# Kernel tuning notes

Hardware: AMD Instinct MI355X
Metric: run time of the kernel (lower is better)

Reference implementation:

```python
import jax, jax.numpy as jnp
import numpy as np
from math import log2

N_QUBITS = 11
N_LAYERS = 2
DEGREE = 3
N_TIMESTEPS = 8
BSZ = 64
DIM = 2 ** N_QUBITS
N_ROTS = 4 * N_QUBITS * N_LAYERS  # 88


def _ry(theta):
    # batched RY(theta): (B,) -> (B,2,2) complex64
    h = 0.5 * theta
    c, s = jnp.cos(h), jnp.sin(h)
    U = jnp.stack([jnp.stack([c, -s], -1), jnp.stack([s, c], -1)], -2)
    return U.astype(jnp.complex64)


def _rx(theta):
    # batched RX(theta): (B,) -> (B,2,2) complex64
    h = 0.5 * theta
    c = jnp.cos(h).astype(jnp.complex64)
    s = (-1j) * jnp.sin(h).astype(jnp.complex64)
    return jnp.stack([jnp.stack([c, s], -1), jnp.stack([s, c], -1)], -2)


def _apply_1q(state, U, w):
    # state: (B,) + (2,)*n ; apply per-batch 2x2 U on wire w
    s = jnp.moveaxis(state, w + 1, 1)
    shp = s.shape
    s = s.reshape(shp[0], 2, -1)
    s = jnp.einsum('bij,bjr->bir', U, s)
    return jnp.moveaxis(s.reshape(shp), 1, w + 1)


def _apply_crx(state, theta, c_w, t_w):
    # controlled-RX: apply RX on target wire t_w where control wire c_w is |1>
    U = _rx(theta)
    s = jnp.moveaxis(state, (c_w + 1, t_w + 1), (1, 2))
    shp = s.shape
    s = s.reshape(shp[0], 2, 2, -1)
    s1 = jnp.einsum('bij,bjr->bir', U, s[:, 1])
    s = jnp.concatenate([s[:, :1], s1[:, None]], axis=1).reshape(shp)
    return jnp.moveaxis(s, (1, 2), (c_w + 1, t_w + 1))


def _sim14_evolve(state, params):
    # faithful sim14_circuit (v3 fixed RY-CRX gate set), batched angles
    n = state.ndim - 1
    layers = params.shape[1] // (4 * n)
    idx = 0
    for _ in range(layers):
        for i in range(n):
            state = _apply_1q(state, _ry(params[:, idx]), i); idx += 1
        for i in range(n - 1, -1, -1):
            state = _apply_crx(state, params[:, idx], i, (i + 1) % n); idx += 1
        for i in range(n):
            state = _apply_1q(state, _ry(params[:, idx]), i); idx += 1
        for i in [n - 1] + list(range(n - 1)):
            state = _apply_crx(state, params[:, idx], i, (i - 1) % n); idx += 1
    return state


def _apply_unitaries(base, uparams, coeffs):
    # apply_unitaries_pl: repeat_interleave + evolve + LCU einsum
    bsz, T, n_rots = uparams.shape
    dim = base.shape[1]
    n = int(round(log2(dim)))
    flat = uparams.reshape(bsz * T, n_rots)
    rep = jnp.repeat(base, T, axis=0).reshape((bsz * T,) + (2,) * n)
    ev = _sim14_evolve(rep, flat).reshape(bsz, T, dim)
    return jnp.einsum('bti,bt->bi', ev, coeffs.astype(jnp.complex64))


def setup_inputs() -> dict:
    key = jax.random.key(0)
    k1, k2, k3, k4 = jax.random.split(key, 4)
    base_states = jax.random.normal(k1, (BSZ, DIM), dtype=jnp.float32)
    unitary_params = jax.random.normal(k2, (BSZ, N_TIMESTEPS, N_ROTS), dtype=jnp.float32)
    lcu_coeffs = jax.random.normal(k3, (BSZ, N_TIMESTEPS), dtype=jnp.float32)
    poly_coeffs = jax.random.normal(k4, (DEGREE + 1,), dtype=jnp.float32)
    return {"base_states": base_states, "unitary_params": unitary_params,
            "lcu_coeffs": lcu_coeffs, "poly_coeffs": poly_coeffs}


def reference(base_states, unitary_params, lcu_coeffs, poly_coeffs):
    # evaluate_polynomial_state_pl (QSVT polynomial state preparation)
    base = base_states.astype(jnp.complex64)
    base = base / jnp.linalg.norm(base, axis=1, keepdims=True)  # valid quantum state
    pc = poly_coeffs.astype(jnp.complex64)
    acc = pc[0] * base
    working = base
    for k in range(1, poly_coeffs.shape[0]):
        working = _apply_unitaries(working, unitary_params, lcu_coeffs)
        acc = acc + pc[k] * working
    out = acc / jnp.sum(jnp.abs(poly_coeffs)).astype(jnp.complex64)
    # return real/imag stacked so output is real-valued: (bsz, dim, 2)
    return jnp.stack([out.real, out.imag], axis=-1)
```

## Files before the change

### kernel.cpp

```cpp
#include <hip/hip_runtime.h>
#include <utility>

#define DIM 2048
#define NQ 11
#define NROT 88
#define BSZ 64
#define NT 8
#define NPC 4

#if __has_builtin(__builtin_amdgcn_permlane16_swap)
#define HAVE_PL16 1
#else
#define HAVE_PL16 0
#endif
#if __has_builtin(__builtin_amdgcn_permlane32_swap)
#define HAVE_PL32 1
#else
#define HAVE_PL32 0
#endif

constexpr int g_type(int G) {
    int j = G % 44;
    return (j < 11 || (j >= 22 && j < 33)) ? 0 : 1;
}
constexpr int g_pt(int G) {
    int j = G % 44;
    if (j < 11) return 10 - j;
    if (j < 22) { int i = 21 - j; int tw = (i + 1 == NQ) ? 0 : i + 1; return 10 - tw; }
    if (j < 33) return 10 - (j - 22);
    if (j == 33) return 1;
    int i = j - 34; int tw = (i + 10) % NQ; return 10 - tw;
}
constexpr int g_pcb(int G) {
    int j = G % 44;
    if (j >= 11 && j < 22) { int i = 21 - j; return 10 - i; }
    if (j == 33) return 0;
    if (j >= 34) { int i = j - 34; return 10 - i; }
    return -1;
}
constexpr bool use_sum_tier(int lb) {
    return (lb == 4 && HAVE_PL16) || (lb == 5 && HAVE_PL32);
}

constexpr int tmap(int b) {
    if (b == 2) return 8;  if (b == 8) return 2;
    if (b == 3) return 9;  if (b == 9) return 3;
    if (b == 5) return 10; if (b == 10) return 5;
    return b;
}

constexpr int lop_j(int k) {
    if (k < 8)  return 3 + k;
    if (k == 8) return -1;
    if (k < 12) return k - 9;
    if (k == 12) return 11;
    if (k == 13) return -1;
    if (k < 22) return 12 + (k - 14);
    if (k == 22) return -1;
    if (k == 23) return 20;
    if (k == 24) return 21;
    if (k < 31) { int w[6] = {0, 1, 2, 3, 9, 10}; return 22 + w[k - 25]; }
    if (k < 36) return 33 + (k - 31);
    if (k == 36) return -1;
    if (k < 42) return 26 + (k - 37);
    return 38 + (k - 42);
}
constexpr bool lop_B(int k) {
    return (k >= 9 && k <= 12) || (k >= 23 && k <= 35);
}
constexpr int lop_tpar(int k) { return (k == 8 || k == 22) ? 0 : 1; }

template<int G>
__device__ __forceinline__ void get_cs(float c0, float s0, float c1, float s1,
                                       float& c, float& s) {
    if constexpr (G < 64) {
        c = __int_as_float(__builtin_amdgcn_readlane(__float_as_int(c0), G));
        s = __int_as_float(__builtin_amdgcn_readlane(__float_as_int(s0), G));
    } else {
        c = __int_as_float(__builtin_amdgcn_readlane(__float_as_int(c1), G - 64));
        s = __int_as_float(__builtin_amdgcn_readlane(__float_as_int(s1), G - 64));
    }
}

template<int LB>
__device__ __forceinline__ float lxp(float x) {
    if constexpr (LB == 0) {
        return __int_as_float(__builtin_amdgcn_update_dpp(
            __float_as_int(x), __float_as_int(x), 0xB1, 0xF, 0xF, true));
    } else if constexpr (LB == 1) {
        return __int_as_float(__builtin_amdgcn_update_dpp(
            __float_as_int(x), __float_as_int(x), 0x4E, 0xF, 0xF, true));
    } else if constexpr (LB == 2) {
        return __int_as_float(__builtin_amdgcn_ds_swizzle(__float_as_int(x), 0x101F));
    } else if constexpr (LB == 3) {
        return __int_as_float(__builtin_amdgcn_update_dpp(
            __float_as_int(x), __float_as_int(x), 0x128, 0xF, 0xF, true));
    } else if constexpr (LB == 4) {
        return __int_as_float(__builtin_amdgcn_ds_swizzle(__float_as_int(x), 0x401F));
    } else {
        return __shfl_xor(x, 32, 64);
    }
}

template<int LB>
__device__ __forceinline__ float lxsum(float x) {
#if HAVE_PL16
    if constexpr (LB == 4) {
        unsigned u = __float_as_uint(x);
        auto r = __builtin_amdgcn_permlane16_swap(u, u, false, false);
        return __uint_as_float(r[0]) + __uint_as_float(r[1]);
    }
#endif
#if HAVE_PL32
    if constexpr (LB == 5) {
        unsigned u = __float_as_uint(x);
        auto r = __builtin_amdgcn_permlane32_swap(u, u, false, false);
        return __uint_as_float(r[0]) + __uint_as_float(r[1]);
    }
#endif
    return x + lxp<LB>(x);
}

template<int G, bool PB>
__device__ __forceinline__ void apply_gate(
    float2 (&R)[2], float2 (&I)[2],
    float c0, float s0, float c1, float s1,
    float4* __restrict__ exbuf, const int tid)
{
    constexpr int type = g_type(G);
    constexpr int pt0  = g_pt(G);
    constexpr int pcb0 = g_pcb(G);
    constexpr int pt   = PB ? tmap(pt0) : pt0;
    constexpr int pcb  = (pcb0 < 0) ? -1 : (PB ? tmap(pcb0) : pcb0);
    float c, s;
    get_cs<G>(c0, s0, c1, s1, c, s);

    if constexpr (pt == 0) {
        if constexpr (type == 0) {
#pragma unroll
            for (int m = 0; m < 2; ++m) {
                float er = R[m].x, orr = R[m].y, ei = I[m].x, oi = I[m].y;
                R[m].x = c*er - s*orr;  R[m].y = s*er + c*orr;
                I[m].x = c*ei - s*oi;   I[m].y = s*ei + c*oi;
            }
        } else if constexpr (pcb == 1) {
            float er = R[1].x, orr = R[1].y, ei = I[1].x, oi = I[1].y;
            R[1].x = c*er + s*oi;   I[1].x = c*ei - s*orr;
            R[1].y = c*orr + s*ei;  I[1].y = c*oi - s*er;
        } else {
            const bool ctrl = (tid >> (pcb - 2)) & 1;
            if (ctrl) {
#pragma unroll
                for (int m = 0; m < 2; ++m) {
                    float er = R[m].x, orr = R[m].y, ei = I[m].x, oi = I[m].y;
                    R[m].x = c*er + s*oi;   I[m].x = c*ei - s*orr;
                    R[m].y = c*orr + s*ei;  I[m].y = c*oi - s*er;
                }
            }
        }
    } else if constexpr (pt == 1) {
        if constexpr (type == 0) {
            float2 l = R[0], h = R[1], li = I[0], hi = I[1];
            R[0].x = c*l.x - s*h.x;   R[0].y = c*l.y - s*h.y;
            R[1].x = s*l.x + c*h.x;   R[1].y = s*l.y + c*h.y;
            I[0].x = c*li.x - s*hi.x; I[0].y = c*li.y - s*hi.y;
            I[1].x = s*li.x + c*hi.x; I[1].y = s*li.y + c*hi.y;
        } else if constexpr (pcb == 0) {
            float lr = R[0].y, li = I[0].y, hr = R[1].y, hi = I[1].y;
            R[0].y = c*lr + s*hi;   I[0].y = c*li - s*hr;
            R[1].y = c*hr + s*li;   I[1].y = c*hi - s*lr;
        } else {
            const bool ctrl = (tid >> (pcb - 2)) & 1;
            if (ctrl) {
                float2 l = R[0], h = R[1], li = I[0], hi = I[1];
                R[0].x = c*l.x + s*hi.x;  R[0].y = c*l.y + s*hi.y;
                I[0].x = c*li.x - s*h.x;  I[0].y = c*li.y - s*h.y;
                R[1].x = c*h.x + s*li.x;  R[1].y = c*h.y + s*li.y;
                I[1].x = c*hi.x - s*l.x;  I[1].y = c*hi.y - s*l.y;
            }
        }
    } else if constexpr (pt <= 7) {
        constexpr int lb = pt - 2;
        if constexpr (use_sum_tier(lb)) {
            if constexpr (type == 0) {
                const float sg = ((tid >> lb) & 1) ? s : -s;
                const float k1 = c - sg;
#pragma unroll
                for (int m = 0; m < 2; ++m) {
                    float srx = lxsum<lb>(R[m].x), sry = lxsum<lb>(R[m].y);
                    float six = lxsum<lb>(I[m].x), siy = lxsum<lb>(I[m].y);
                    R[m].x = k1*R[m].x + sg*srx;  R[m].y = k1*R[m].y + sg*sry;
                    I[m].x = k1*I[m].x + sg*six;  I[m].y = k1*I[m].y + sg*siy;
                }
            } else if constexpr (pcb == 0) {
#pragma unroll
                for (int m = 0; m < 2; ++m) {
                    float sR = lxsum<lb>(R[m].y), sI = lxsum<lb>(I[m].y);
                    float r = R[m].y, i = I[m].y;
                    R[m].y = c*r - s*i + s*sI;
                    I[m].y = c*i + s*r - s*sR;
                }
            } else if constexpr (pcb == 1) {
                float sRx = lxsum<lb>(R[1].x), sRy = lxsum<lb>(R[1].y);
                float sIx = lxsum<lb>(I[1].x), sIy = lxsum<lb>(I[1].y);
                float rx = R[1].x, ry = R[1].y, ix = I[1].x, iy = I[1].y;
                R[1].x = c*rx - s*ix + s*sIx;  R[1].y = c*ry - s*iy + s*sIy;
                I[1].x = c*ix + s*rx - s*sRx;  I[1].y = c*iy + s*ry - s*sRy;
            } else {
                const bool ctrl = (tid >> (pcb - 2)) & 1;
                if (ctrl) {
#pragma unroll
                    for (int m = 0; m < 2; ++m) {
                        float sRx = lxsum<lb>(R[m].x), sRy = lxsum<lb>(R[m].y);
                        float sIx = lxsum<lb>(I[m].x), sIy = lxsum<lb>(I[m].y);
                        float rx = R[m].x, ry = R[m].y, ix = I[m].x, iy = I[m].y;
                        R[m].x = c*rx - s*ix + s*sIx;  R[m].y = c*ry - s*iy + s*sIy;
                        I[m].x = c*ix + s*rx - s*sRx;  I[m].y = c*iy + s*ry - s*sRy;
                    }
                }
            }
        } else {
            if constexpr (type == 0) {
                const float sg = ((tid >> lb) & 1) ? s : -s;
#pragma unroll
                for (int m = 0; m < 2; ++m) {
                    float prx = lxp<lb>(R[m].x), pry = lxp<lb>(R[m].y);
                    float pix = lxp<lb>(I[m].x), piy = lxp<lb>(I[m].y);
                    R[m].x = c*R[m].x + sg*prx;  R[m].y = c*R[m].y + sg*pry;
                    I[m].x = c*I[m].x + sg*pix;  I[m].y = c*I[m].y + sg*piy;
                }
            } else if constexpr (pcb == 0) {
#pragma unroll
                for (int m = 0; m < 2; ++m) {
                    float pry = lxp<lb>(R[m].y), piy = lxp<lb>(I[m].y);
                    R[m].y = c*R[m].y + s*piy;
                    I[m].y = c*I[m].y - s*pry;
                }
            } else if constexpr (pcb == 1) {
                float prx = lxp<lb>(R[1].x), pry = lxp<lb>(R[1].y);
                float pix = lxp<lb>(I[1].x), piy = lxp<lb>(I[1].y);
                R[1].x = c*R[1].x + s*pix;  R[1].y = c*R[1].y + s*piy;
                I[1].x = c*I[1].x - s*prx;  I[1].y = c*I[1].y - s*pry;
            } else {
                const bool ctrl = (tid >> (pcb - 2)) & 1;
                if (ctrl) {
#pragma unroll
                    for (int m = 0; m < 2; ++m) {
                        float prx = lxp<lb>(R[m].x), pry = lxp<lb>(R[m].y);
                        float pix = lxp<lb>(I[m].x), piy = lxp<lb>(I[m].y);
                        R[m].x = c*R[m].x + s*pix;  R[m].y = c*R[m].y + s*piy;
                        I[m].x = c*I[m].x - s*prx;  I[m].y = c*I[m].y - s*pry;
                    }
                }
            }
        }
    }
}

__device__ __forceinline__ int swz(int s) { return s ^ ((s >> 7) & 7); }

template<int PAR>
__device__ __forceinline__ void transpose_swap(float2 (&R)[2], float2 (&I)[2],
                                               float4* __restrict__ exbuf, const int tid)
{
    float4* buf = exbuf + PAR * 1024;
    const int d06 = ((tid >> 0) ^ (tid >> 6)) & 1;
    const int d17 = ((tid >> 1) ^ (tid >> 7)) & 1;
    const int d38 = ((tid >> 3) ^ (tid >> 8)) & 1;
    const int q = tid ^ (d06 * 65) ^ (d17 * 130) ^ (d38 * 264);
    buf[swz(tid * 2 + 0)] = make_float4(R[0].x, R[0].y, I[0].x, I[0].y);
    buf[swz(tid * 2 + 1)] = make_float4(R[1].x, R[1].y, I[1].x, I[1].y);
    __syncthreads();
    float4 v0 = buf[swz(q * 2 + 0)];
    float4 v1 = buf[swz(q * 2 + 1)];
    R[0] = make_float2(v0.x, v0.y); I[0] = make_float2(v0.z, v0.w);
    R[1] = make_float2(v1.x, v1.y); I[1] = make_float2(v1.z, v1.w);
}

template<int K>
__device__ __forceinline__ void apply_op(
    float2 (&R)[2], float2 (&I)[2],
    float c0, float s0, float c1, float s1,
    float4* __restrict__ exbuf, const int tid)
{
    constexpr int layer = K / 48;
    constexpr int k = K % 48;
    constexpr int j = lop_j(k);
    if constexpr (j < 0) {
        transpose_swap<lop_tpar(k)>(R, I, exbuf, tid);
    } else {
        apply_gate<layer * 44 + j, lop_B(k)>(R, I, c0, s0, c1, s1, exbuf, tid);
    }
}

template<int... Ks>
__device__ __forceinline__ void apply_all(std::integer_sequence<int, Ks...>,
    float2 (&R)[2], float2 (&I)[2],
    float c0, float s0, float c1, float s1,
    float4* __restrict__ exbuf, const int tid)
{
    (apply_op<Ks>(R, I, c0, s0, c1, s1, exbuf, tid), ...);
}

template<int MODE>
__global__ __launch_bounds__(512, 4) void evolve_kernel(
    const void* __restrict__ src, const float* __restrict__ uparams,
    const float* __restrict__ lcu, float2* __restrict__ pout,
    const float* __restrict__ pcoef, float2* __restrict__ acc, int kprev)
{
    __shared__ float4 exbuf[2048];
    __shared__ float red[9];

    const int b = blockIdx.x >> 3;
    const int t = blockIdx.x & 7;
    const int tid = threadIdx.x;
    const int lane = tid & 63;

    const float* __restrict__ th_row = uparams + (size_t)(b * NT + t) * NROT;
    float th0 = 0.5f * th_row[lane];
    float th1 = (lane < NROT - 64) ? 0.5f * th_row[64 + lane] : 0.f;
    float tc0 = cosf(th0), ts0 = sinf(th0);
    float tc1 = cosf(th1), ts1 = sinf(th1);

    float2 R[2], I[2];
    if constexpr (MODE == 0) {
        const float4* b4 = (const float4*)((const float*)src + (size_t)b * DIM);
        float4 v = b4[tid];
        float loc = v.x*v.x + v.y*v.y + v.z*v.z + v.w*v.w;
        for (int off = 32; off > 0; off >>= 1) loc += __shfl_down(loc, off, 64);
        if ((tid & 63) == 0) red[tid >> 6] = loc;
        __syncthreads();
        if (tid == 0) { float sm = 0.f; for (int w = 0; w < 8; ++w) sm += red[w]; red[8] = sm; }
        __syncthreads();
        const float inv = rsqrtf(red[8]);
        R[0] = make_float2(v.x * inv, v.y * inv);
        R[1] = make_float2(v.z * inv, v.w * inv);
        I[0] = make_float2(0.f, 0.f);
        I[1] = make_float2(0.f, 0.f);
        if (t == 0) {
            const float p0 = pcoef[0];
            float4* a4 = (float4*)(acc + (size_t)b * DIM);
            a4[tid*2+0] = make_float4(p0*R[0].x, 0.f, p0*R[0].y, 0.f);
            a4[tid*2+1] = make_float4(p0*R[1].x, 0.f, p0*R[1].y, 0.f);
        }
    } else if constexpr (MODE == 1) {
        R[0] = R[1] = I[0] = I[1] = make_float2(0.f, 0.f);
        const float2* s2 = (const float2*)src;
        for (int cc = 0; cc < NT; ++cc) {
            const float4* p4 = (const float4*)(s2 + ((size_t)b * NT + cc) * DIM);
#pragma unroll
            for (int m = 0; m < 2; ++m) {
                float4 v = p4[tid*2+m];
                R[m].x += v.x; I[m].x += v.y; R[m].y += v.z; I[m].y += v.w;
            }
        }
        if (t == 0) {
            const float pk = pcoef[kprev];
            float4* a4 = (float4*)(acc + (size_t)b * DIM);
#pragma unroll
            for (int m = 0; m < 2; ++m) {
                float4 v = a4[tid*2+m];
                v.x += pk * R[m].x; v.y += pk * I[m].x;
                v.z += pk * R[m].y; v.w += pk * I[m].y;
                a4[tid*2+m] = v;
            }
        }
    } else {
        const float2* s2 = (const float2*)src;
        const float4* p4 = (const float4*)(s2 + (size_t)b * DIM);
#pragma unroll
        for (int m = 0; m < 2; ++m) {
            float4 v = p4[tid*2+m];
            R[m].x = v.x; I[m].x = v.y; R[m].y = v.z; I[m].y = v.w;
        }
    }

    apply_all(std::make_integer_sequence<int, 96>{}, R, I,
              tc0, ts0, tc1, ts1, exbuf, tid);

    const float coeff = lcu[b * NT + t];
    float4* o4 = (float4*)(pout + ((size_t)b * NT + t) * DIM);
#pragma unroll
    for (int m = 0; m < 2; ++m)
        o4[tid*2+m] = make_float4(coeff*R[m].x, coeff*I[m].x, coeff*R[m].y, coeff*I[m].y);
}

__global__ __launch_bounds__(256) void final_kernel(
    const float2* __restrict__ partial, const float* __restrict__ pcoef,
    const float2* __restrict__ acc, float* __restrict__ out)
{
    int b = blockIdx.x >> 3;
    int i = ((blockIdx.x & 7) << 8) | threadIdx.x;
    float sr = 0.f, si = 0.f;
    for (int c = 0; c < NT; ++c) {
        float2 v = partial[((size_t)b * NT + c) * DIM + i];
        sr += v.x; si += v.y;
    }
    float sabs = 0.f;
    for (int q = 0; q < NPC; ++q) sabs += fabsf(pcoef[q]);
    float invn = 1.0f / sabs;
    float pk = pcoef[NPC - 1];
    float2 a = acc[(size_t)b * DIM + i];
    out[((size_t)b * DIM + i) * 2 + 0] = (a.x + pk * sr) * invn;
    out[((size_t)b * DIM + i) * 2 + 1] = (a.y + pk * si) * invn;
}

__global__ __launch_bounds__(256) void setup_kernel(
    const float* __restrict__ base, const float* __restrict__ pc,
    float2* __restrict__ working, float2* __restrict__ acc)
{
    int b = blockIdx.x;
    int tid = threadIdx.x;
    __shared__ float red[4];
    float ssum = 0.f;
    for (int i = tid; i < DIM; i += 256) {
        float v = base[b * DIM + i];
        ssum += v * v;
    }
    for (int off = 32; off > 0; off >>= 1) ssum += __shfl_down(ssum, off, 64);
    if ((tid & 63) == 0) red[tid >> 6] = ssum;
    __syncthreads();
    if (tid == 0) red[0] = red[0] + red[1] + red[2] + red[3];
    __syncthreads();
    float inv = rsqrtf(red[0]);
    float p0 = pc[0];
    for (int i = tid; i < DIM; i += 256) {
        float v = base[b * DIM + i] * inv;
        working[b * DIM + i] = make_float2(v, 0.f);
        acc[b * DIM + i] = make_float2(p0 * v, 0.f);
    }
}

__global__ __launch_bounds__(256) void reduce_kernel(
    const float2* __restrict__ partial, const float* __restrict__ pcoef,
    float2* __restrict__ working, float2* __restrict__ acc,
    float* __restrict__ out, int k, int last)
{
    int b = blockIdx.x >> 3;
    int i = ((blockIdx.x & 7) << 8) | threadIdx.x;
    float pk = pcoef[k];
    float sr = 0.f, si = 0.f;
    for (int c = 0; c < NT; ++c) {
        float2 v = partial[((size_t)b * NT + c) * DIM + i];
        sr += v.x; si += v.y;
    }
    working[b * DIM + i] = make_float2(sr, si);
    float2 a = acc[b * DIM + i];
    a.x += pk * sr; a.y += pk * si;
    acc[b * DIM + i] = a;
    if (last) {
        float sabs = 0.f;
        for (int q = 0; q < NPC; ++q) sabs += fabsf(pcoef[q]);
        float invn = 1.0f / sabs;
        out[((size_t)b * DIM + i) * 2 + 0] = a.x * invn;
        out[((size_t)b * DIM + i) * 2 + 1] = a.y * invn;
    }
}

extern "C" void kernel_launch(void* const* d_in, const int* in_sizes, int n_in,
                              void* d_out, int out_size, void* d_ws, size_t ws_size,
                              hipStream_t stream) {
    const float* base = (const float*)d_in[0];
    const float* upar = (const float*)d_in[1];
    const float* lcu  = (const float*)d_in[2];
    const float* pc   = (const float*)d_in[3];
    float* out = (float*)d_out;

    const size_t plane = (size_t)BSZ * DIM * sizeof(float2);
    char* ws = (char*)d_ws;

    if (ws_size >= (1 + 3 * (size_t)NT) * plane) {
        float2* acc = (float2*)ws;
        float2* pA  = (float2*)(ws + plane);
        float2* pB  = (float2*)(ws + plane + (size_t)NT * plane);
        float2* pC  = (float2*)(ws + plane + (size_t)2 * NT * plane);
        evolve_kernel<0><<<BSZ * NT, 512, 0, stream>>>(base, upar, lcu, pA, pc, acc, 0);
        evolve_kernel<1><<<BSZ * NT, 512, 0, stream>>>(pA,   upar, lcu, pB, pc, acc, 1);
        evolve_kernel<1><<<BSZ * NT, 512, 0, stream>>>(pB,   upar, lcu, pC, pc, acc, 2);
        final_kernel<<<BSZ * 8, 256, 0, stream>>>(pC, pc, acc, out);
    } else {
        float2* working = (float2*)ws;
        float2* acc     = (float2*)(ws + plane);
        float2* pA      = (float2*)(ws + 2 * plane);
        setup_kernel<<<BSZ, 256, 0, stream>>>(base, pc, working, acc);
        for (int k = 1; k <= NPC - 1; ++k) {
            evolve_kernel<2><<<BSZ * NT, 512, 0, stream>>>(working, upar, lcu, pA, pc, acc, 0);
            reduce_kernel<<<BSZ * 8, 256, 0, stream>>>(pA, pc, working, acc, out,
                                                       k, (k == NPC - 1) ? 1 : 0);
        }
    }
}
```

Baseline: 85.24 us.

## Use 1024 threads per state with one amplitude pair each and 4-bit transposes

Each evolve block now runs 1024 threads, each holding one complex pair instead of two. The qubit-to-lane mapping, the transpose schedule (now three shared-memory transposes per layer with a 16-way swizzle) and the gate dispatch are all rebuilt to match. The aim is more parallelism per state and less register pressure per thread, so cross-lane gate work gets spread over more wavefronts. The cost is an extra transpose and barrier per layer, plus more block-wide synchronisation across 16 waves.

```diff
diff --git a/kernel.cpp b/kernel.cpp
--- a/kernel.cpp
+++ b/kernel.cpp
@@ -43,32 +43,37 @@
 }
 
 constexpr int tmap(int b) {
-    if (b == 2) return 8;  if (b == 8) return 2;
-    if (b == 3) return 9;  if (b == 9) return 3;
-    if (b == 5) return 10; if (b == 10) return 5;
+    if (b >= 1 && b <= 4) return b + 6;
+    if (b >= 7 && b <= 10) return b - 6;
     return b;
 }
 
 constexpr int lop_j(int k) {
-    if (k < 8)  return 3 + k;
-    if (k == 8) return -1;
-    if (k < 12) return k - 9;
+    if (k < 7)  return 4 + k;
+    if (k == 7) return -1;
+    if (k < 12) return k - 8;
     if (k == 12) return 11;
     if (k == 13) return -1;
-    if (k < 22) return 12 + (k - 14);
-    if (k == 22) return -1;
-    if (k == 23) return 20;
-    if (k == 24) return 21;
-    if (k < 31) { int w[6] = {0, 1, 2, 3, 9, 10}; return 22 + w[k - 25]; }
-    if (k < 36) return 33 + (k - 31);
-    if (k == 36) return -1;
-    if (k < 42) return 26 + (k - 37);
-    return 38 + (k - 42);
+    if (k < 21) return 12 + (k - 14);
+    if (k == 21) return -1;
+    if (k < 25) return 19 + (k - 22);
+    if (k < 29) return 22 + (k - 25);
+    if (k == 29) return 26;
+    if (k == 30) return 27;
+    if (k == 31) return 32;
+    if (k == 32) return -1;
+    if (k < 37) return 28 + (k - 33);
+    if (k == 37) return 33;
+    if (k == 38) return 34;
+    if (k == 39) return -1;
+    if (k < 46) return 35 + (k - 40);
+    if (k == 46) return -1;
+    return 41 + (k - 47);
 }
 constexpr bool lop_B(int k) {
-    return (k >= 9 && k <= 12) || (k >= 23 && k <= 35);
-}
-constexpr int lop_tpar(int k) { return (k == 8 || k == 22) ? 0 : 1; }
+    return (k >= 8 && k <= 12) || (k >= 22 && k <= 31) || (k >= 40 && k <= 45);
+}
+constexpr int lop_tpar(int k) { return (k == 7 || k == 21 || k == 39) ? 0 : 1; }
 
 template<int G>
 __device__ __forceinline__ void get_cs(float c0, float s0, float c1, float s1,
@@ -122,180 +127,114 @@
 }
 
 template<int G, bool PB>
-__device__ __forceinline__ void apply_gate(
-    float2 (&R)[2], float2 (&I)[2],
-    float c0, float s0, float c1, float s1,
-    float4* __restrict__ exbuf, const int tid)
+__device__ __forceinline__ void apply_gate(float2& R, float2& I,
+    float c0, float s0, float c1, float s1, const int tid)
 {
     constexpr int type = g_type(G);
-    constexpr int pt0  = g_pt(G);
+    constexpr int pt   = PB ? tmap(g_pt(G)) : g_pt(G);
     constexpr int pcb0 = g_pcb(G);
-    constexpr int pt   = PB ? tmap(pt0) : pt0;
     constexpr int pcb  = (pcb0 < 0) ? -1 : (PB ? tmap(pcb0) : pcb0);
+    static_assert(pt <= 6, "block-bit target must run in transposed layout");
     float c, s;
     get_cs<G>(c0, s0, c1, s1, c, s);
 
     if constexpr (pt == 0) {
         if constexpr (type == 0) {
-#pragma unroll
-            for (int m = 0; m < 2; ++m) {
-                float er = R[m].x, orr = R[m].y, ei = I[m].x, oi = I[m].y;
-                R[m].x = c*er - s*orr;  R[m].y = s*er + c*orr;
-                I[m].x = c*ei - s*oi;   I[m].y = s*ei + c*oi;
+            float rx = R.x, ry = R.y, ix = I.x, iy = I.y;
+            R.x = c*rx - s*ry;  R.y = s*rx + c*ry;
+            I.x = c*ix - s*iy;  I.y = s*ix + c*iy;
+        } else {
+            const bool ctrl = (tid >> (pcb - 1)) & 1;
+            if (ctrl) {
+                float rx = R.x, ry = R.y, ix = I.x, iy = I.y;
+                R.x = c*rx + s*iy;   I.x = c*ix - s*ry;
+                R.y = c*ry + s*ix;   I.y = c*iy - s*rx;
             }
-        } else if constexpr (pcb == 1) {
-            float er = R[1].x, orr = R[1].y, ei = I[1].x, oi = I[1].y;
-            R[1].x = c*er + s*oi;   I[1].x = c*ei - s*orr;
-            R[1].y = c*orr + s*ei;  I[1].y = c*oi - s*er;
-        } else {
-            const bool ctrl = (tid >> (pcb - 2)) & 1;
-            if (ctrl) {
-#pragma unroll
-                for (int m = 0; m < 2; ++m) {
-                    float er = R[m].x, orr = R[m].y, ei = I[m].x, oi = I[m].y;
-                    R[m].x = c*er + s*oi;   I[m].x = c*ei - s*orr;
-                    R[m].y = c*orr + s*ei;  I[m].y = c*oi - s*er;
-                }
-            }
-        }
-    } else if constexpr (pt == 1) {
-        if constexpr (type == 0) {
-            float2 l = R[0], h = R[1], li = I[0], hi = I[1];
-            R[0].x = c*l.x - s*h.x;   R[0].y = c*l.y - s*h.y;
-            R[1].x = s*l.x + c*h.x;   R[1].y = s*l.y + c*h.y;
-            I[0].x = c*li.x - s*hi.x; I[0].y = c*li.y - s*hi.y;
-            I[1].x = s*li.x + c*hi.x; I[1].y = s*li.y + c*hi.y;
-        } else if constexpr (pcb == 0) {
-            float lr = R[0].y, li = I[0].y, hr = R[1].y, hi = I[1].y;
-            R[0].y = c*lr + s*hi;   I[0].y = c*li - s*hr;
-            R[1].y = c*hr + s*li;   I[1].y = c*hi - s*lr;
-        } else {
-            const bool ctrl = (tid >> (pcb - 2)) & 1;
-            if (ctrl) {
-                float2 l = R[0], h = R[1], li = I[0], hi = I[1];
-                R[0].x = c*l.x + s*hi.x;  R[0].y = c*l.y + s*hi.y;
-                I[0].x = c*li.x - s*h.x;  I[0].y = c*li.y - s*h.y;
-                R[1].x = c*h.x + s*li.x;  R[1].y = c*h.y + s*li.y;
-                I[1].x = c*hi.x - s*l.x;  I[1].y = c*hi.y - s*l.y;
-            }
-        }
-    } else if constexpr (pt <= 7) {
-        constexpr int lb = pt - 2;
+        }
+    } else {
+        constexpr int lb = pt - 1;
         if constexpr (use_sum_tier(lb)) {
             if constexpr (type == 0) {
                 const float sg = ((tid >> lb) & 1) ? s : -s;
                 const float k1 = c - sg;
-#pragma unroll
-                for (int m = 0; m < 2; ++m) {
-                    float srx = lxsum<lb>(R[m].x), sry = lxsum<lb>(R[m].y);
-                    float six = lxsum<lb>(I[m].x), siy = lxsum<lb>(I[m].y);
-                    R[m].x = k1*R[m].x + sg*srx;  R[m].y = k1*R[m].y + sg*sry;
-                    I[m].x = k1*I[m].x + sg*six;  I[m].y = k1*I[m].y + sg*siy;
-                }
+                float srx = lxsum<lb>(R.x), sry = lxsum<lb>(R.y);
+                float six = lxsum<lb>(I.x), siy = lxsum<lb>(I.y);
+                R.x = k1*R.x + sg*srx;  R.y = k1*R.y + sg*sry;
+                I.x = k1*I.x + sg*six;  I.y = k1*I.y + sg*siy;
             } else if constexpr (pcb == 0) {
-#pragma unroll
-                for (int m = 0; m < 2; ++m) {
-                    float sR = lxsum<lb>(R[m].y), sI = lxsum<lb>(I[m].y);
-                    float r = R[m].y, i = I[m].y;
-                    R[m].y = c*r - s*i + s*sI;
-                    I[m].y = c*i + s*r - s*sR;
-                }
-            } else if constexpr (pcb == 1) {
-                float sRx = lxsum<lb>(R[1].x), sRy = lxsum<lb>(R[1].y);
-                float sIx = lxsum<lb>(I[1].x), sIy = lxsum<lb>(I[1].y);
-                float rx = R[1].x, ry = R[1].y, ix = I[1].x, iy = I[1].y;
-                R[1].x = c*rx - s*ix + s*sIx;  R[1].y = c*ry - s*iy + s*sIy;
-                I[1].x = c*ix + s*rx - s*sRx;  I[1].y = c*iy + s*ry - s*sRy;
+                float sry = lxsum<lb>(R.y), siy = lxsum<lb>(I.y);
+                float ry = R.y, iy = I.y;
+                R.y = c*ry - s*iy + s*siy;
+                I.y = c*iy + s*ry - s*sry;
             } else {
-                const bool ctrl = (tid >> (pcb - 2)) & 1;
+                const bool ctrl = (tid >> (pcb - 1)) & 1;
                 if (ctrl) {
-#pragma unroll
-                    for (int m = 0; m < 2; ++m) {
-                        float sRx = lxsum<lb>(R[m].x), sRy = lxsum<lb>(R[m].y);
-                        float sIx = lxsum<lb>(I[m].x), sIy = lxsum<lb>(I[m].y);
-                        float rx = R[m].x, ry = R[m].y, ix = I[m].x, iy = I[m].y;
-                        R[m].x = c*rx - s*ix + s*sIx;  R[m].y = c*ry - s*iy + s*sIy;
-                        I[m].x = c*ix + s*rx - s*sRx;  I[m].y = c*iy + s*ry - s*sRy;
-                    }
+                    float srx = lxsum<lb>(R.x), sry = lxsum<lb>(R.y);
+                    float six = lxsum<lb>(I.x), siy = lxsum<lb>(I.y);
+                    float rx = R.x, ry = R.y, ix = I.x, iy = I.y;
+                    R.x = c*rx - s*ix + s*six;  R.y = c*ry - s*iy + s*siy;
+                    I.x = c*ix + s*rx - s*srx;  I.y = c*iy + s*ry - s*sry;
                 }
             }
         } else {
             if constexpr (type == 0) {
                 const float sg = ((tid >> lb) & 1) ? s : -s;
-#pragma unroll
-                for (int m = 0; m < 2; ++m) {
-                    float prx = lxp<lb>(R[m].x), pry = lxp<lb>(R[m].y);
-                    float pix = lxp<lb>(I[m].x), piy = lxp<lb>(I[m].y);
-                    R[m].x = c*R[m].x + sg*prx;  R[m].y = c*R[m].y + sg*pry;
-                    I[m].x = c*I[m].x + sg*pix;  I[m].y = c*I[m].y + sg*piy;
-                }
+                float prx = lxp<lb>(R.x), pry = lxp<lb>(R.y);
+                float pix = lxp<lb>(I.x), piy = lxp<lb>(I.y);
+                R.x = c*R.x + sg*prx;  R.y = c*R.y + sg*pry;
+                I.x = c*I.x + sg*pix;  I.y = c*I.y + sg*piy;
             } else if constexpr (pcb == 0) {
-#pragma unroll
-                for (int m = 0; m < 2; ++m) {
-                    float pry = lxp<lb>(R[m].y), piy = lxp<lb>(I[m].y);
-                    R[m].y = c*R[m].y + s*piy;
-                    I[m].y = c*I[m].y - s*pry;
-                }
-            } else if constexpr (pcb == 1) {
-                float prx = lxp<lb>(R[1].x), pry = lxp<lb>(R[1].y);
-                float pix = lxp<lb>(I[1].x), piy = lxp<lb>(I[1].y);
-                R[1].x = c*R[1].x + s*pix;  R[1].y = c*R[1].y + s*piy;
-                I[1].x = c*I[1].x - s*prx;  I[1].y = c*I[1].y - s*pry;
+                float pry = lxp<lb>(R.y), piy = lxp<lb>(I.y);
+                R.y = c*R.y + s*piy;
+                I.y = c*I.y - s*pry;
             } else {
-                const bool ctrl = (tid >> (pcb - 2)) & 1;
+                const bool ctrl = (tid >> (pcb - 1)) & 1;
                 if (ctrl) {
-#pragma unroll
-                    for (int m = 0; m < 2; ++m) {
-                        float prx = lxp<lb>(R[m].x), pry = lxp<lb>(R[m].y);
-                        float pix = lxp<lb>(I[m].x), piy = lxp<lb>(I[m].y);
-                        R[m].x = c*R[m].x + s*pix;  R[m].y = c*R[m].y + s*piy;
-                        I[m].x = c*I[m].x - s*prx;  I[m].y = c*I[m].y - s*pry;
-                    }
+                    float prx = lxp<lb>(R.x), pry = lxp<lb>(R.y);
+                    float pix = lxp<lb>(I.x), piy = lxp<lb>(I.y);
+                    R.x = c*R.x + s*pix;  R.y = c*R.y + s*piy;
+                    I.x = c*I.x - s*prx;  I.y = c*I.y - s*pry;
                 }
             }
         }
     }
 }
 
-__device__ __forceinline__ int swz(int s) { return s ^ ((s >> 7) & 7); }
+__device__ __forceinline__ int swz16(int s) { return s ^ ((s >> 6) & 15); }
 
 template<int PAR>
-__device__ __forceinline__ void transpose_swap(float2 (&R)[2], float2 (&I)[2],
-                                               float4* __restrict__ exbuf, const int tid)
+__device__ __forceinline__ void transpose_swap(float2& R, float2& I,
+    float4* __restrict__ exbuf, const int tid)
 {
     float4* buf = exbuf + PAR * 1024;
-    const int d06 = ((tid >> 0) ^ (tid >> 6)) & 1;
-    const int d17 = ((tid >> 1) ^ (tid >> 7)) & 1;
-    const int d38 = ((tid >> 3) ^ (tid >> 8)) & 1;
-    const int q = tid ^ (d06 * 65) ^ (d17 * 130) ^ (d38 * 264);
-    buf[swz(tid * 2 + 0)] = make_float4(R[0].x, R[0].y, I[0].x, I[0].y);
-    buf[swz(tid * 2 + 1)] = make_float4(R[1].x, R[1].y, I[1].x, I[1].y);
+    const int lo = tid & 15;
+    const int hi = (tid >> 6) & 15;
+    const int q = (tid & 0x030) | hi | (lo << 6);
+    buf[swz16(tid)] = make_float4(R.x, R.y, I.x, I.y);
     __syncthreads();
-    float4 v0 = buf[swz(q * 2 + 0)];
-    float4 v1 = buf[swz(q * 2 + 1)];
-    R[0] = make_float2(v0.x, v0.y); I[0] = make_float2(v0.z, v0.w);
-    R[1] = make_float2(v1.x, v1.y); I[1] = make_float2(v1.z, v1.w);
+    float4 v = buf[swz16(q)];
+    R = make_float2(v.x, v.y);
+    I = make_float2(v.z, v.w);
 }
 
 template<int K>
-__device__ __forceinline__ void apply_op(
-    float2 (&R)[2], float2 (&I)[2],
+__device__ __forceinline__ void apply_op(float2& R, float2& I,
     float c0, float s0, float c1, float s1,
     float4* __restrict__ exbuf, const int tid)
 {
-    constexpr int layer = K / 48;
-    constexpr int k = K % 48;
+    constexpr int layer = K / 50;
+    constexpr int k = K % 50;
     constexpr int j = lop_j(k);
     if constexpr (j < 0) {
         transpose_swap<lop_tpar(k)>(R, I, exbuf, tid);
     } else {
-        apply_gate<layer * 44 + j, lop_B(k)>(R, I, c0, s0, c1, s1, exbuf, tid);
+        apply_gate<layer * 44 + j, lop_B(k)>(R, I, c0, s0, c1, s1, tid);
     }
 }
 
 template<int... Ks>
 __device__ __forceinline__ void apply_all(std::integer_sequence<int, Ks...>,
-    float2 (&R)[2], float2 (&I)[2],
+    float2& R, float2& I,
     float c0, float s0, float c1, float s1,
     float4* __restrict__ exbuf, const int tid)
 {
@@ -303,13 +242,13 @@
 }
 
 template<int MODE>
-__global__ __launch_bounds__(512, 4) void evolve_kernel(
+__global__ __launch_bounds__(1024, 8) void evolve_kernel(
     const void* __restrict__ src, const float* __restrict__ uparams,
     const float* __restrict__ lcu, float2* __restrict__ pout,
     const float* __restrict__ pcoef, float2* __restrict__ acc, int kprev)
 {
     __shared__ float4 exbuf[2048];
-    __shared__ float red[9];
+    __shared__ float red[16];
 
     const int b = blockIdx.x >> 3;
     const int t = blockIdx.x & 7;
@@ -322,67 +261,54 @@
     float tc0 = cosf(th0), ts0 = sinf(th0);
     float tc1 = cosf(th1), ts1 = sinf(th1);
 
-    float2 R[2], I[2];
+    float2 R, I;
     if constexpr (MODE == 0) {
-        const float4* b4 = (const float4*)((const float*)src + (size_t)b * DIM);
-        float4 v = b4[tid];
-        float loc = v.x*v.x + v.y*v.y + v.z*v.z + v.w*v.w;
+        const float2* b2s = (const float2*)((const float*)src + (size_t)b * DIM);
+        float2 v = b2s[tid];
+        float loc = v.x * v.x + v.y * v.y;
         for (int off = 32; off > 0; off >>= 1) loc += __shfl_down(loc, off, 64);
-        if ((tid & 63) == 0) red[tid >> 6] = loc;
+        if (lane == 0) red[tid >> 6] = loc;
         __syncthreads();
-        if (tid == 0) { float sm = 0.f; for (int w = 0; w < 8; ++w) sm += red[w]; red[8] = sm; }
-        __syncthreads();
-        const float inv = rsqrtf(red[8]);
-        R[0] = make_float2(v.x * inv, v.y * inv);
-        R[1] = make_float2(v.z * inv, v.w * inv);
-        I[0] = make_float2(0.f, 0.f);
-        I[1] = make_float2(0.f, 0.f);
+        float tot = 0.f;
+#pragma unroll
+        for (int w = 0; w < 16; ++w) tot += red[w];
+        const float inv = rsqrtf(tot);
+        R = make_float2(v.x * inv, v.y * inv);
+        I = make_float2(0.f, 0.f);
         if (t == 0) {
             const float p0 = pcoef[0];
             float4* a4 = (float4*)(acc + (size_t)b * DIM);
-            a4[tid*2+0] = make_float4(p0*R[0].x, 0.f, p0*R[0].y, 0.f);
-            a4[tid*2+1] = make_float4(p0*R[1].x, 0.f, p0*R[1].y, 0.f);
+            a4[tid] = make_float4(p0 * R.x, 0.f, p0 * R.y, 0.f);
         }
     } else if constexpr (MODE == 1) {
-        R[0] = R[1] = I[0] = I[1] = make_float2(0.f, 0.f);
+        R = make_float2(0.f, 0.f); I = make_float2(0.f, 0.f);
         const float2* s2 = (const float2*)src;
         for (int cc = 0; cc < NT; ++cc) {
             const float4* p4 = (const float4*)(s2 + ((size_t)b * NT + cc) * DIM);
-#pragma unroll
-            for (int m = 0; m < 2; ++m) {
-                float4 v = p4[tid*2+m];
-                R[m].x += v.x; I[m].x += v.y; R[m].y += v.z; I[m].y += v.w;
-            }
+            float4 v = p4[tid];
+            R.x += v.x; I.x += v.y; R.y += v.z; I.y += v.w;
         }
         if (t == 0) {
             const float pk = pcoef[kprev];
             float4* a4 = (float4*)(acc + (size_t)b * DIM);
-#pragma unroll
-            for (int m = 0; m < 2; ++m) {
-                float4 v = a4[tid*2+m];
-                v.x += pk * R[m].x; v.y += pk * I[m].x;
-                v.z += pk * R[m].y; v.w += pk * I[m].y;
-                a4[tid*2+m] = v;
-            }
+            float4 v = a4[tid];
+            v.x += pk * R.x; v.y += pk * I.x;
+            v.z += pk * R.y; v.w += pk * I.y;
+            a4[tid] = v;
         }
     } else {
         const float2* s2 = (const float2*)src;
         const float4* p4 = (const float4*)(s2 + (size_t)b * DIM);
-#pragma unroll
-        for (int m = 0; m < 2; ++m) {
-            float4 v = p4[tid*2+m];
-            R[m].x = v.x; I[m].x = v.y; R[m].y = v.z; I[m].y = v.w;
-        }
-    }
-
-    apply_all(std::make_integer_sequence<int, 96>{}, R, I,
+        float4 v = p4[tid];
+        R.x = v.x; I.x = v.y; R.y = v.z; I.y = v.w;
+    }
+
+    apply_all(std::make_integer_sequence<int, 100>{}, R, I,
               tc0, ts0, tc1, ts1, exbuf, tid);
 
     const float coeff = lcu[b * NT + t];
     float4* o4 = (float4*)(pout + ((size_t)b * NT + t) * DIM);
-#pragma unroll
-    for (int m = 0; m < 2; ++m)
-        o4[tid*2+m] = make_float4(coeff*R[m].x, coeff*I[m].x, coeff*R[m].y, coeff*I[m].y);
+    o4[tid] = make_float4(coeff * R.x, coeff * I.x, coeff * R.y, coeff * I.y);
 }
 
 __global__ __launch_bounds__(256) void final_kernel(
@@ -474,9 +400,9 @@
         float2* pA  = (float2*)(ws + plane);
         float2* pB  = (float2*)(ws + plane + (size_t)NT * plane);
         float2* pC  = (float2*)(ws + plane + (size_t)2 * NT * plane);
-        evolve_kernel<0><<<BSZ * NT, 512, 0, stream>>>(base, upar, lcu, pA, pc, acc, 0);
-        evolve_kernel<1><<<BSZ * NT, 512, 0, stream>>>(pA,   upar, lcu, pB, pc, acc, 1);
-        evolve_kernel<1><<<BSZ * NT, 512, 0, stream>>>(pB,   upar, lcu, pC, pc, acc, 2);
+        evolve_kernel<0><<<BSZ * NT, 1024, 0, stream>>>(base, upar, lcu, pA, pc, acc, 0);
+        evolve_kernel<1><<<BSZ * NT, 1024, 0, stream>>>(pA,   upar, lcu, pB, pc, acc, 1);
+        evolve_kernel<1><<<BSZ * NT, 1024, 0, stream>>>(pB,   upar, lcu, pC, pc, acc, 2);
         final_kernel<<<BSZ * 8, 256, 0, stream>>>(pC, pc, acc, out);
     } else {
         float2* working = (float2*)ws;
@@ -484,7 +410,7 @@
         float2* pA      = (float2*)(ws + 2 * plane);
         setup_kernel<<<BSZ, 256, 0, stream>>>(base, pc, working, acc);
         for (int k = 1; k <= NPC - 1; ++k) {
-            evolve_kernel<2><<<BSZ * NT, 512, 0, stream>>>(working, upar, lcu, pA, pc, acc, 0);
+            evolve_kernel<2><<<BSZ * NT, 1024, 0, stream>>>(working, upar, lcu, pA, pc, acc, 0);
             reduce_kernel<<<BSZ * 8, 256, 0, stream>>>(pA, pc, working, acc, out,
                                                        k, (k == NPC - 1) ? 1 : 0);
         }
```

Result: slower. 90.75 us (+6.5%).

## Fuse final reduction into last evolve kernel and use DPP fused-multiply-add gates

Applied to the files above, without the earlier changes.

Removes the separate final reduction kernel. The last evolve kernel now uses a per-batch atomic counter so the last-finishing block sums the eight partials, adds the accumulator and writes the normalized output. It also adds inline-asm v_fmac_f32_dpp paths that fuse the lane exchange with the multiply-add for the permute-tier gates at lane distances 1, 2 and 8. This saves a kernel launch and some instructions per gate, at the cost of a memset, an atomic, a threadfence, and a serialized tail in which a single block per batch reads all partials.

```diff
diff --git a/kernel.cpp b/kernel.cpp
--- a/kernel.cpp
+++ b/kernel.cpp
@@ -103,6 +103,20 @@
 }
 
 template<int LB>
+__device__ __forceinline__ void fmac_dpp(float& acc, float src, float coef) {
+    if constexpr (LB == 0) {
+        asm("v_fmac_f32_dpp %0, %2, %3 quad_perm:[1,0,3,2] row_mask:0xf bank_mask:0xf"
+            : "=v"(acc) : "0"(acc), "v"(src), "v"(coef));
+    } else if constexpr (LB == 1) {
+        asm("v_fmac_f32_dpp %0, %2, %3 quad_perm:[2,3,0,1] row_mask:0xf bank_mask:0xf"
+            : "=v"(acc) : "0"(acc), "v"(src), "v"(coef));
+    } else {
+        asm("v_fmac_f32_dpp %0, %2, %3 row_ror:8 row_mask:0xf bank_mask:0xf"
+            : "=v"(acc) : "0"(acc), "v"(src), "v"(coef));
+    }
+}
+
+template<int LB>
 __device__ __forceinline__ float lxsum(float x) {
 #if HAVE_PL16
     if constexpr (LB == 4) {
@@ -124,14 +138,13 @@
 template<int G, bool PB>
 __device__ __forceinline__ void apply_gate(
     float2 (&R)[2], float2 (&I)[2],
-    float c0, float s0, float c1, float s1,
-    float4* __restrict__ exbuf, const int tid)
+    float c0, float s0, float c1, float s1, const int tid)
 {
     constexpr int type = g_type(G);
-    constexpr int pt0  = g_pt(G);
+    constexpr int pt   = PB ? tmap(g_pt(G)) : g_pt(G);
     constexpr int pcb0 = g_pcb(G);
-    constexpr int pt   = PB ? tmap(pt0) : pt0;
     constexpr int pcb  = (pcb0 < 0) ? -1 : (PB ? tmap(pcb0) : pcb0);
+    static_assert(pt <= 7, "block-bit target must run in transposed layout");
     float c, s;
     get_cs<G>(c0, s0, c1, s1, c, s);
 
@@ -179,8 +192,9 @@
                 I[1].x = c*hi.x - s*l.x;  I[1].y = c*hi.y - s*l.y;
             }
         }
-    } else if constexpr (pt <= 7) {
+    } else {
         constexpr int lb = pt - 2;
+        constexpr bool dppable = (lb == 0 || lb == 1 || lb == 3);
         if constexpr (use_sum_tier(lb)) {
             if constexpr (type == 0) {
                 const float sg = ((tid >> lb) & 1) ? s : -s;
@@ -216,6 +230,46 @@
                         float rx = R[m].x, ry = R[m].y, ix = I[m].x, iy = I[m].y;
                         R[m].x = c*rx - s*ix + s*sIx;  R[m].y = c*ry - s*iy + s*sIy;
                         I[m].x = c*ix + s*rx - s*sRx;  I[m].y = c*iy + s*ry - s*sRy;
+                    }
+                }
+            }
+        } else if constexpr (dppable) {
+            if constexpr (type == 0) {
+                const float sgn = ((tid >> lb) & 1) ? s : -s;
+#pragma unroll
+                for (int m = 0; m < 2; ++m) {
+                    float nrx = c*R[m].x; fmac_dpp<lb>(nrx, R[m].x, sgn);
+                    float nry = c*R[m].y; fmac_dpp<lb>(nry, R[m].y, sgn);
+                    float nix = c*I[m].x; fmac_dpp<lb>(nix, I[m].x, sgn);
+                    float niy = c*I[m].y; fmac_dpp<lb>(niy, I[m].y, sgn);
+                    R[m].x = nrx; R[m].y = nry; I[m].x = nix; I[m].y = niy;
+                }
+            } else if constexpr (pcb == 0) {
+                const float vs = s, vns = -s;
+#pragma unroll
+                for (int m = 0; m < 2; ++m) {
+                    float nry = c*R[m].y; fmac_dpp<lb>(nry, I[m].y, vs);
+                    float niy = c*I[m].y; fmac_dpp<lb>(niy, R[m].y, vns);
+                    R[m].y = nry; I[m].y = niy;
+                }
+            } else if constexpr (pcb == 1) {
+                const float vs = s, vns = -s;
+                float nrx = c*R[1].x; fmac_dpp<lb>(nrx, I[1].x, vs);
+                float nry = c*R[1].y; fmac_dpp<lb>(nry, I[1].y, vs);
+                float nix = c*I[1].x; fmac_dpp<lb>(nix, R[1].x, vns);
+                float niy = c*I[1].y; fmac_dpp<lb>(niy, R[1].y, vns);
+                R[1].x = nrx; R[1].y = nry; I[1].x = nix; I[1].y = niy;
+            } else {
+                const bool ctrl = (tid >> (pcb - 2)) & 1;
+                if (ctrl) {
+                    const float vs = s, vns = -s;
+#pragma unroll
+                    for (int m = 0; m < 2; ++m) {
+                        float nrx = c*R[m].x; fmac_dpp<lb>(nrx, I[m].x, vs);
+                        float nry = c*R[m].y; fmac_dpp<lb>(nry, I[m].y, vs);
+                        float nix = c*I[m].x; fmac_dpp<lb>(nix, R[m].x, vns);
+                        float niy = c*I[m].y; fmac_dpp<lb>(niy, R[m].y, vns);
+                        R[m].x = nrx; R[m].y = nry; I[m].x = nix; I[m].y = niy;
                     }
                 }
             }
@@ -289,7 +343,7 @@
     if constexpr (j < 0) {
         transpose_swap<lop_tpar(k)>(R, I, exbuf, tid);
     } else {
-        apply_gate<layer * 44 + j, lop_B(k)>(R, I, c0, s0, c1, s1, exbuf, tid);
+        apply_gate<layer * 44 + j, lop_B(k)>(R, I, c0, s0, c1, s1, tid);
     }
 }
 
@@ -302,14 +356,23 @@
     (apply_op<Ks>(R, I, c0, s0, c1, s1, exbuf, tid), ...);
 }
 
-template<int MODE>
+__device__ __forceinline__ void evolve_once(float2 (&R)[2], float2 (&I)[2],
+    float c0, float s0, float c1, float s1,
+    float4* __restrict__ exbuf, const int tid)
+{
+    apply_all(std::make_integer_sequence<int, 96>{}, R, I, c0, s0, c1, s1, exbuf, tid);
+}
+
+template<int MODE, bool DO_FINAL>
 __global__ __launch_bounds__(512, 4) void evolve_kernel(
     const void* __restrict__ src, const float* __restrict__ uparams,
     const float* __restrict__ lcu, float2* __restrict__ pout,
-    const float* __restrict__ pcoef, float2* __restrict__ acc, int kprev)
+    const float* __restrict__ pcoef, float2* __restrict__ acc, int kprev,
+    int* __restrict__ cnt, float* __restrict__ out)
 {
     __shared__ float4 exbuf[2048];
     __shared__ float red[9];
+    __shared__ int sLast;
 
     const int b = blockIdx.x >> 3;
     const int t = blockIdx.x & 7;
@@ -343,8 +406,10 @@
             a4[tid*2+0] = make_float4(p0*R[0].x, 0.f, p0*R[0].y, 0.f);
             a4[tid*2+1] = make_float4(p0*R[1].x, 0.f, p0*R[1].y, 0.f);
         }
-    } else if constexpr (MODE == 1) {
-        R[0] = R[1] = I[0] = I[1] = make_float2(0.f, 0.f);
+        __syncthreads();
+    } else {
+        R[0] = make_float2(0.f, 0.f); R[1] = make_float2(0.f, 0.f);
+        I[0] = make_float2(0.f, 0.f); I[1] = make_float2(0.f, 0.f);
         const float2* s2 = (const float2*)src;
         for (int cc = 0; cc < NT; ++cc) {
             const float4* p4 = (const float4*)(s2 + ((size_t)b * NT + cc) * DIM);
@@ -354,7 +419,7 @@
                 R[m].x += v.x; I[m].x += v.y; R[m].y += v.z; I[m].y += v.w;
             }
         }
-        if (t == 0) {
+        if (t == 0 && kprev > 0) {
             const float pk = pcoef[kprev];
             float4* a4 = (float4*)(acc + (size_t)b * DIM);
 #pragma unroll
@@ -365,95 +430,45 @@
                 a4[tid*2+m] = v;
             }
         }
-    } else {
-        const float2* s2 = (const float2*)src;
-        const float4* p4 = (const float4*)(s2 + (size_t)b * DIM);
-#pragma unroll
-        for (int m = 0; m < 2; ++m) {
-            float4 v = p4[tid*2+m];
-            R[m].x = v.x; I[m].x = v.y; R[m].y = v.z; I[m].y = v.w;
-        }
-    }
-
-    apply_all(std::make_integer_sequence<int, 96>{}, R, I,
-              tc0, ts0, tc1, ts1, exbuf, tid);
+    }
+
+    evolve_once(R, I, tc0, ts0, tc1, ts1, exbuf, tid);
 
     const float coeff = lcu[b * NT + t];
     float4* o4 = (float4*)(pout + ((size_t)b * NT + t) * DIM);
 #pragma unroll
     for (int m = 0; m < 2; ++m)
         o4[tid*2+m] = make_float4(coeff*R[m].x, coeff*I[m].x, coeff*R[m].y, coeff*I[m].y);
-}
-
-__global__ __launch_bounds__(256) void final_kernel(
-    const float2* __restrict__ partial, const float* __restrict__ pcoef,
-    const float2* __restrict__ acc, float* __restrict__ out)
-{
-    int b = blockIdx.x >> 3;
-    int i = ((blockIdx.x & 7) << 8) | threadIdx.x;
-    float sr = 0.f, si = 0.f;
-    for (int c = 0; c < NT; ++c) {
-        float2 v = partial[((size_t)b * NT + c) * DIM + i];
-        sr += v.x; si += v.y;
-    }
-    float sabs = 0.f;
-    for (int q = 0; q < NPC; ++q) sabs += fabsf(pcoef[q]);
-    float invn = 1.0f / sabs;
-    float pk = pcoef[NPC - 1];
-    float2 a = acc[(size_t)b * DIM + i];
-    out[((size_t)b * DIM + i) * 2 + 0] = (a.x + pk * sr) * invn;
-    out[((size_t)b * DIM + i) * 2 + 1] = (a.y + pk * si) * invn;
-}
-
-__global__ __launch_bounds__(256) void setup_kernel(
-    const float* __restrict__ base, const float* __restrict__ pc,
-    float2* __restrict__ working, float2* __restrict__ acc)
-{
-    int b = blockIdx.x;
-    int tid = threadIdx.x;
-    __shared__ float red[4];
-    float ssum = 0.f;
-    for (int i = tid; i < DIM; i += 256) {
-        float v = base[b * DIM + i];
-        ssum += v * v;
-    }
-    for (int off = 32; off > 0; off >>= 1) ssum += __shfl_down(ssum, off, 64);
-    if ((tid & 63) == 0) red[tid >> 6] = ssum;
-    __syncthreads();
-    if (tid == 0) red[0] = red[0] + red[1] + red[2] + red[3];
-    __syncthreads();
-    float inv = rsqrtf(red[0]);
-    float p0 = pc[0];
-    for (int i = tid; i < DIM; i += 256) {
-        float v = base[b * DIM + i] * inv;
-        working[b * DIM + i] = make_float2(v, 0.f);
-        acc[b * DIM + i] = make_float2(p0 * v, 0.f);
-    }
-}
-
-__global__ __launch_bounds__(256) void reduce_kernel(
-    const float2* __restrict__ partial, const float* __restrict__ pcoef,
-    float2* __restrict__ working, float2* __restrict__ acc,
-    float* __restrict__ out, int k, int last)
-{
-    int b = blockIdx.x >> 3;
-    int i = ((blockIdx.x & 7) << 8) | threadIdx.x;
-    float pk = pcoef[k];
-    float sr = 0.f, si = 0.f;
-    for (int c = 0; c < NT; ++c) {
-        float2 v = partial[((size_t)b * NT + c) * DIM + i];
-        sr += v.x; si += v.y;
-    }
-    working[b * DIM + i] = make_float2(sr, si);
-    float2 a = acc[b * DIM + i];
-    a.x += pk * sr; a.y += pk * si;
-    acc[b * DIM + i] = a;
-    if (last) {
-        float sabs = 0.f;
-        for (int q = 0; q < NPC; ++q) sabs += fabsf(pcoef[q]);
-        float invn = 1.0f / sabs;
-        out[((size_t)b * DIM + i) * 2 + 0] = a.x * invn;
-        out[((size_t)b * DIM + i) * 2 + 1] = a.y * invn;
+
+    if constexpr (DO_FINAL) {
+        __threadfence();
+        __syncthreads();
+        if (tid == 0) {
+            int old = __hip_atomic_fetch_add(&cnt[b], 1, __ATOMIC_ACQ_REL,
+                                             __HIP_MEMORY_SCOPE_AGENT);
+            sLast = (old == NT - 1) ? 1 : 0;
+        }
+        __syncthreads();
+        if (sLast) {
+            __threadfence();
+            float sabs = 0.f;
+            for (int q = 0; q < NPC; ++q) sabs += fabsf(pcoef[q]);
+            const float invn = 1.0f / sabs;
+            const float pk = pcoef[NPC - 1];
+            float4* outv = (float4*)(out + (size_t)b * DIM * 2);
+            const float4* accv = (const float4*)(acc + (size_t)b * DIM);
+#pragma unroll
+            for (int jj = tid; jj < DIM / 2; jj += 512) {
+                float4 sum = make_float4(0.f, 0.f, 0.f, 0.f);
+                for (int cc = 0; cc < NT; ++cc) {
+                    float4 v = ((const float4*)(pout + ((size_t)b * NT + cc) * DIM))[jj];
+                    sum.x += v.x; sum.y += v.y; sum.z += v.z; sum.w += v.w;
+                }
+                float4 a = accv[jj];
+                outv[jj] = make_float4((a.x + pk*sum.x) * invn, (a.y + pk*sum.y) * invn,
+                                       (a.z + pk*sum.z) * invn, (a.w + pk*sum.w) * invn);
+            }
+        }
     }
 }
 
@@ -467,26 +482,33 @@
     float* out = (float*)d_out;
 
     const size_t plane = (size_t)BSZ * DIM * sizeof(float2);
+    const size_t cnt_bytes = (size_t)BSZ * sizeof(int);
     char* ws = (char*)d_ws;
 
-    if (ws_size >= (1 + 3 * (size_t)NT) * plane) {
-        float2* acc = (float2*)ws;
-        float2* pA  = (float2*)(ws + plane);
-        float2* pB  = (float2*)(ws + plane + (size_t)NT * plane);
-        float2* pC  = (float2*)(ws + plane + (size_t)2 * NT * plane);
-        evolve_kernel<0><<<BSZ * NT, 512, 0, stream>>>(base, upar, lcu, pA, pc, acc, 0);
-        evolve_kernel<1><<<BSZ * NT, 512, 0, stream>>>(pA,   upar, lcu, pB, pc, acc, 1);
-        evolve_kernel<1><<<BSZ * NT, 512, 0, stream>>>(pB,   upar, lcu, pC, pc, acc, 2);
-        final_kernel<<<BSZ * 8, 256, 0, stream>>>(pC, pc, acc, out);
-    } else {
-        float2* working = (float2*)ws;
-        float2* acc     = (float2*)(ws + plane);
-        float2* pA      = (float2*)(ws + 2 * plane);
-        setup_kernel<<<BSZ, 256, 0, stream>>>(base, pc, working, acc);
-        for (int k = 1; k <= NPC - 1; ++k) {
-            evolve_kernel<2><<<BSZ * NT, 512, 0, stream>>>(working, upar, lcu, pA, pc, acc, 0);
-            reduce_kernel<<<BSZ * 8, 256, 0, stream>>>(pA, pc, working, acc, out,
-                                                       k, (k == NPC - 1) ? 1 : 0);
-        }
-    }
-}
+    float2* acc = (float2*)ws;
+    float2* pA  = (float2*)(ws + plane);
+    float2* pB  = (float2*)(ws + plane + (size_t)NT * plane);
+    float2* pC  = (float2*)(ws + plane + (size_t)2 * NT * plane);
+    int* cnt    = (int*)(ws + plane + (size_t)3 * NT * plane);
+
+    if (ws_size >= (1 + 3 * (size_t)NT) * plane + cnt_bytes) {
+        hipMemsetAsync(cnt, 0, cnt_bytes, stream);
+        evolve_kernel<0, false><<<BSZ * NT, 512, 0, stream>>>(
+            base, upar, lcu, pA, pc, acc, 0, nullptr, nullptr);
+        evolve_kernel<1, false><<<BSZ * NT, 512, 0, stream>>>(
+            pA, upar, lcu, pB, pc, acc, 1, nullptr, nullptr);
+        evolve_kernel<1, true><<<BSZ * NT, 512, 0, stream>>>(
+            pB, upar, lcu, pC, pc, acc, 2, cnt, out);
+    } else {
+        float2* qA = (float2*)(ws + plane);
+        float2* qB = (float2*)(ws + plane + (size_t)NT * plane);
+        int* c2    = (int*)(ws + plane + (size_t)2 * NT * plane);
+        hipMemsetAsync(c2, 0, cnt_bytes, stream);
+        evolve_kernel<0, false><<<BSZ * NT, 512, 0, stream>>>(
+            base, upar, lcu, qA, pc, acc, 0, nullptr, nullptr);
+        evolve_kernel<1, false><<<BSZ * NT, 512, 0, stream>>>(
+            qA, upar, lcu, qB, pc, acc, 1, nullptr, nullptr);
+        evolve_kernel<1, true><<<BSZ * NT, 512, 0, stream>>>(
+            qB, upar, lcu, qA, pc, acc, 2, c2, out);
+    }
+}
```

Result: slower. 245.6 us (+188.2%).
